# Kernel tuning notes

Measured on AMD Instinct MI355X. Metric: run time of the kernel, lower is better.

Reference implementation:

```python
import jax, jax.numpy as jnp
import numpy as np
from jax import lax

B, T_IN, T_TGT = 256, 512, 256
N_IN, N_PV, H, EMB, N_SC = 64, 16, 256, 32, 4

def gru_cell(x, h, Wih, Whh, bih, bhh):
    # PyTorch GRU cell, gate order (r, z, n)
    gi = x @ Wih.T + bih
    gh = h @ Whh.T + bhh
    ir, iz, inn = jnp.split(gi, 3, axis=-1)
    hr, hz, hn = jnp.split(gh, 3, axis=-1)
    r = jax.nn.sigmoid(ir + hr)
    z = jax.nn.sigmoid(iz + hz)
    n = jnp.tanh(inn + r * hn)
    return (1.0 - z) * n + z * h

def setup_inputs() -> dict:
    key = jax.random.key(0)
    ks = jax.random.split(key, 24)
    s = 0.05
    d = {}
    d['x_cv'] = jax.random.normal(ks[0], (B, T_IN, N_IN), jnp.float32)
    d['x_cv_target'] = jax.random.normal(ks[1], (B, T_TGT, N_IN), jnp.float32)
    d['pv_init'] = jax.random.normal(ks[2], (B, N_PV), jnp.float32)
    d['scenario'] = jax.random.randint(ks[3], (B,), 0, N_SC)
    d['emb_table'] = jax.random.normal(ks[4], (N_SC, EMB), jnp.float32) * s
    i = 5
    for name, in0 in (('enc', N_IN + EMB), ('dec', N_IN + N_PV)):
        for l in range(2):
            din = in0 if l == 0 else H
            d[f'{name}_Wih{l}'] = jax.random.normal(ks[i], (3 * H, din), jnp.float32) * s; i += 1
            d[f'{name}_Whh{l}'] = jax.random.normal(ks[i], (3 * H, H), jnp.float32) * s; i += 1
            d[f'{name}_bih{l}'] = jnp.zeros((3 * H,), jnp.float32)
            d[f'{name}_bhh{l}'] = jnp.zeros((3 * H,), jnp.float32)
    d['fc1_W'] = jax.random.normal(ks[i], (128, H), jnp.float32) * s; i += 1
    d['fc1_b'] = jnp.zeros((128,), jnp.float32)
    d['fc2_W'] = jax.random.normal(ks[i], (N_PV, 128), jnp.float32) * s; i += 1
    d['fc2_b'] = jnp.zeros((N_PV,), jnp.float32)
    return d

def reference(x_cv, x_cv_target, pv_init, scenario, emb_table,
              enc_Wih0, enc_Whh0, enc_bih0, enc_bhh0,
              enc_Wih1, enc_Whh1, enc_bih1, enc_bhh1,
              dec_Wih0, dec_Whh0, dec_bih0, dec_bhh0,
              dec_Wih1, dec_Whh1, dec_bih1, dec_bhh1,
              fc1_W, fc1_b, fc2_W, fc2_b):
    b = x_cv.shape[0]
    # Encoder: concat scenario embedding onto each input step, 2-layer GRU
    emb = emb_table[scenario]                              # (B, EMB)
    emb_bt = jnp.broadcast_to(emb[:, None, :], (b, x_cv.shape[1], emb.shape[-1]))
    enc_x = jnp.concatenate([x_cv, emb_bt], axis=-1)       # (B, T_in, N_IN+EMB)
    h_init = (jnp.zeros((b, H), x_cv.dtype), jnp.zeros((b, H), x_cv.dtype))

    def enc_step(carry, xt):
        h0, h1 = carry
        h0 = gru_cell(xt, h0, enc_Wih0, enc_Whh0, enc_bih0, enc_bhh0)
        h1 = gru_cell(h0, h1, enc_Wih1, enc_Whh1, enc_bih1, enc_bhh1)
        return (h0, h1), None

    (h0, h1), _ = lax.scan(enc_step, h_init, enc_x.transpose(1, 0, 2))

    def dec_step(carry, xt):
        d0, d1, pv = carry
        din = jnp.concatenate([xt, pv], axis=-1)           # (B, N_IN+N_PV)
        d0 = gru_cell(din, d0, dec_Wih0, dec_Whh0, dec_bih0, dec_bhh0)
        d1 = gru_cell(d0, d1, dec_Wih1, dec_Whh1, dec_bih1, dec_bhh1)
        y = jax.nn.relu(d1 @ fc1_W.T + fc1_b) @ fc2_W.T + fc2_b  # (B, N_PV)
        return (d0, d1, y), y

    _, ys = lax.scan(dec_step, (h0, h1, pv_init), x_cv_target.transpose(1, 0, 2))
    return ys.transpose(1, 0, 2)                           # (B, T_tgt, N_PV)
```

## Files before the change

### kernel.cpp

```cpp
#include <hip/hip_runtime.h>


typedef _Float16 f16x8 __attribute__((ext_vector_type(8)));
typedef float f32x4 __attribute__((ext_vector_type(4)));

#define XSTR 104
#define HSTR 264
#define YSTR 136

#define OFF_E0IH 0u
#define OFF_E0HH 73728u
#define OFF_E1IH 270336u
#define OFF_E1HH 466944u
#define OFF_D0IH 663552u
#define OFF_D0HH 737280u
#define OFF_D1IH 933888u
#define OFF_D1HH 1130496u
#define OFF_FC1  1327104u
#define OFF_FC2  1359872u
#define W_TOTAL_F16 1361920u
#define BIAS_BYTE_OFF 2723840u
#define EXCH_BYTE_OFF 2740224u
#define EX_H0 0
#define EX_H1 262144
#define EX_PV 524288
#define EX_FLAGS 532480
#define EX_BYTES 567296

__device__ __forceinline__ float sigm(float x) { return 1.f / (1.f + __expf(-x)); }
__device__ __forceinline__ float tanh_fast(float x) { return 1.f - 2.f / (__expf(2.f * x) + 1.f); }

__device__ __forceinline__ f32x4 mfma(f16x8 a, f16x8 b, f32x4 c) {
    return __builtin_amdgcn_mfma_f32_16x16x32_f16(a, b, c, 0, 0, 0);
}

__device__ __forceinline__ void store_coh_f16(_Float16* p, _Float16 v) {
    union { _Float16 h; unsigned short u; } cv; cv.h = v;
    unsigned int ui = cv.u;
    asm volatile("global_store_short %0, %1, off sc0 sc1" :: "v"(p), "v"(ui) : "memory");
}
__device__ __forceinline__ unsigned short load_coh_u16(const _Float16* p) {
    unsigned int r;
    asm volatile("global_load_ushort %0, %1, off sc0 sc1\n\ts_waitcnt vmcnt(0)"
                 : "=v"(r) : "v"(p) : "memory");
    return (unsigned short)r;
}

__device__ __forceinline__ void stage_h(const _Float16* src, _Float16* dst, int tid) {
    if (tid < 256) {
        int row = tid >> 4, c = tid & 15;
        const _Float16* p = src + (size_t)row * 256 + c * 16;
        f16x8 a, b;
        asm volatile(
            "global_load_dwordx4 %0, %2, off sc0 sc1\n\t"
            "global_load_dwordx4 %1, %2, off offset:16 sc0 sc1\n\t"
            "s_waitcnt vmcnt(0)"
            : "=v"(a), "=v"(b) : "v"(p) : "memory");
        *(f16x8*)(dst + row * HSTR + c * 16) = a;
        *(f16x8*)(dst + row * HSTR + c * 16 + 8) = b;
    }
}
__device__ __forceinline__ void stage_h2(const _Float16* s0, const _Float16* s1,
                                         _Float16* d0, _Float16* d1, int tid) {
    if (tid < 256) {
        int row = tid >> 4, c = tid & 15;
        const _Float16* p0 = s0 + (size_t)row * 256 + c * 16;
        const _Float16* p1 = s1 + (size_t)row * 256 + c * 16;
        f16x8 a, b, e, f;
        asm volatile(
            "global_load_dwordx4 %0, %4, off sc0 sc1\n\t"
            "global_load_dwordx4 %1, %4, off offset:16 sc0 sc1\n\t"
            "global_load_dwordx4 %2, %5, off sc0 sc1\n\t"
            "global_load_dwordx4 %3, %5, off offset:16 sc0 sc1\n\t"
            "s_waitcnt vmcnt(0)"
            : "=v"(a), "=v"(b), "=v"(e), "=v"(f) : "v"(p0), "v"(p1) : "memory");
        *(f16x8*)(d0 + row * HSTR + c * 16) = a;
        *(f16x8*)(d0 + row * HSTR + c * 16 + 8) = b;
        *(f16x8*)(d1 + row * HSTR + c * 16) = e;
        *(f16x8*)(d1 + row * HSTR + c * 16 + 8) = f;
    }
}

__global__ __launch_bounds__(256) void prep_w(const float* __restrict__ W,
                                              _Float16* __restrict__ dst,
                                              int K_src, int GT, int total_threads) {
    int idx = blockIdx.x * 256 + threadIdx.x;
    if (idx >= total_threads) return;
    int l = idx & 63, c = idx >> 6;
    int kt = c / GT, gt = c - kt * GT;
    int g = gt * 16 + (l & 15);
    int k0 = kt * 32 + (l >> 4) * 8;
    _Float16 tmp[8];
#pragma unroll
    for (int j = 0; j < 8; ++j) {
        int k = k0 + j;
        tmp[j] = (k < K_src) ? (_Float16)W[(size_t)g * K_src + k] : (_Float16)0.f;
    }
    *(f16x8*)(dst + (size_t)c * 512 + (size_t)l * 8) = *(f16x8*)tmp;
}

__global__ __launch_bounds__(256) void prep_bias(const float* __restrict__ bih,
                                                 const float* __restrict__ bhh,
                                                 float* __restrict__ dst) {
    int i = threadIdx.x;
    dst[i]       = bih[i]       + bhh[i];
    dst[256 + i] = bih[256 + i] + bhh[256 + i];
    dst[512 + i] = bih[512 + i];
    dst[768 + i] = bhh[512 + i];
}

template <int KT>
__device__ __forceinline__ f32x4 mmk(const _Float16* ap, const f16x8 (&B)[8]) {
    f32x4 acc = {0.f, 0.f, 0.f, 0.f};
#pragma unroll
    for (int kt = 0; kt < KT; ++kt)
        acc = mfma(*(const f16x8*)(ap + kt * 32), B[kt], acc);
    return acc;
}

__device__ __forceinline__ void h_update(const float* Gb, float* HM,
                                         _Float16* hex_slice, int l,
                                         float bR, float bZ, float bNi, float bNh) {
#pragma unroll
    for (int i = 0; i < 4; ++i) {
        int row = (l >> 4) * 4 + i, col = l & 15;
        int rc = row * 17 + col;
        float r = sigm(Gb[rc] + bR);
        float z = sigm(Gb[272 + rc] + bZ);
        float n = tanh_fast(Gb[2 * 272 + rc] + bNi + r * (Gb[3 * 272 + rc] + bNh));
        float hp = HM[row * 16 + col];
        float hn = (1.f - z) * n + z * hp;
        HM[row * 16 + col] = hn;
        store_coh_f16(hex_slice + (size_t)row * 256 + col, (_Float16)hn);
    }
}

__global__ __launch_bounds__(384, 2) void plant(
    const float* __restrict__ x_cv, const float* __restrict__ x_tgt,
    const float* __restrict__ pv_init, const int* __restrict__ scen,
    const float* __restrict__ emb,
    const _Float16* __restrict__ Wsw, const float* __restrict__ bias4,
    const float* __restrict__ fc1b, const float* __restrict__ fc2b,
    char* __restrict__ exch, float* __restrict__ out)
{
    __shared__ _Float16 XF[16 * XSTR];
    __shared__ _Float16 HA0[16 * HSTR];
    __shared__ _Float16 HA1[16 * HSTR];
    __shared__ _Float16 YF[16 * YSTR];
    __shared__ float G[2][4][272];
    __shared__ float H0M[256], H1M[256];

    const int tid = threadIdx.x;
    const int l = tid & 63, w = tid >> 6;
    const int g = blockIdx.x >> 4, cg = blockIdx.x & 15;
    const int g16 = g * 16;
    const int j = (w < 3) ? w : w - 3;
    const int gt = j * 16 + cg;

    _Float16* h0ex = (_Float16*)(exch + EX_H0);
    _Float16* h1ex = (_Float16*)(exch + EX_H1);
    _Float16* pvex = (_Float16*)(exch + EX_PV);
    int* gflags = (int*)(exch + EX_FLAGS) + g * (17 * 32);
    int* pvflag = gflags + 16 * 32;

    const int arow = l & 15, acol8 = (l >> 4) * 8;
    const size_t slice_off = (size_t)g16 * 256 + cg * 16;
    const _Float16* XFp = XF + arow * XSTR + acol8;
    const _Float16* HA0p = HA0 + arow * HSTR + acol8;
    const _Float16* HA1p = HA1 + arow * HSTR + acol8;

    int ticket = 0;
    auto barrier = [&](int target) {
        __syncthreads();
        if (w == 0) {
            if (l == 0)
                __hip_atomic_store(&gflags[cg * 32], target, __ATOMIC_RELAXED,
                                   __HIP_MEMORY_SCOPE_AGENT);
            if (l < 16)
                while (__hip_atomic_load(&gflags[l * 32], __ATOMIC_RELAXED,
                                         __HIP_MEMORY_SCOPE_AGENT) < target)
                    __builtin_amdgcn_s_sleep(1);
        }
        __syncthreads();
    };

    for (int i = tid; i < 256; i += 384) { H0M[i] = 0.f; H1M[i] = 0.f; }
    if (tid < 256) {
        int row = tid >> 4, c2 = (tid & 15) * 2;
        int sc = scen[g16 + row];
        XF[row * XSTR + 64 + c2]     = (_Float16)emb[sc * 32 + c2];
        XF[row * XSTR + 64 + c2 + 1] = (_Float16)emb[sc * 32 + c2 + 1];
    }

    f16x8 Bx[8], Bh[8];
    {
        unsigned offi = (w < 3) ? OFF_E0IH : OFF_E1IH;
        unsigned offh = (w < 3) ? OFF_E0HH : OFF_E1HH;
        int ktx = (w < 3) ? 3 : 8;
#pragma unroll
        for (int kt = 0; kt < 8; ++kt) {
            if (kt < ktx) Bx[kt] = *(const f16x8*)(Wsw + offi + (size_t)(kt * 48 + gt) * 512 + l * 8);
            Bh[kt] = *(const f16x8*)(Wsw + offh + (size_t)(kt * 48 + gt) * 512 + l * 8);
        }
    }
    float bR = 0.f, bZ = 0.f, bNi = 0.f, bNh = 0.f;
    {
        const float* bb = (w == 0) ? bias4 : bias4 + 1024;
        int hc = cg * 16 + (l & 15);
        if (w == 0 || w == 3) { bR = bb[hc]; bZ = bb[256 + hc]; bNi = bb[512 + hc]; bNh = bb[768 + hc]; }
    }

    float4 xpre;
    const float* xsrc0 = x_cv + (size_t)(g16 + (tid >> 4)) * (512 * 64) + (tid & 15) * 4;
    if (tid < 256) xpre = *(const float4*)xsrc0;
    __syncthreads();

    for (int t = 0; t <= 512; ++t) {
        if (t < 512 && tid < 256) {
            int row = tid >> 4, c4 = (tid & 15) * 4;
            XF[row * XSTR + c4]     = (_Float16)xpre.x;
            XF[row * XSTR + c4 + 1] = (_Float16)xpre.y;
            XF[row * XSTR + c4 + 2] = (_Float16)xpre.z;
            XF[row * XSTR + c4 + 3] = (_Float16)xpre.w;
        }
        stage_h2(h0ex + (size_t)((t - 1) & 1) * 65536 + (size_t)g16 * 256,
                 h1ex + (size_t)(t & 1) * 65536 + (size_t)g16 * 256, HA0, HA1, tid);
        __syncthreads();
        if (tid < 256 && t + 1 < 512) xpre = *(const float4*)(xsrc0 + (size_t)(t + 1) * 64);

        bool doL0 = (w < 3) && (t < 512);
        bool doL1 = (w >= 3) && (t > 0);
        if (doL0 || doL1) {
            f32x4 accX, accH;
            if (doL0) { accX = mmk<3>(XFp, Bx);  accH = mmk<8>(HA0p, Bh); }
            else      { accX = mmk<8>(HA0p, Bx); accH = mmk<8>(HA1p, Bh); }
            float* Gb = &G[(w < 3) ? 0 : 1][0][0];
#pragma unroll
            for (int i = 0; i < 4; ++i) {
                int rc = ((l >> 4) * 4 + i) * 17 + (l & 15);
                if (j < 2) Gb[j * 272 + rc] = accX[i] + accH[i];
                else { Gb[2 * 272 + rc] = accX[i]; Gb[3 * 272 + rc] = accH[i]; }
            }
        }
        __syncthreads();
        if (w == 0 && t < 512)
            h_update(&G[0][0][0], H0M, h0ex + (size_t)(t & 1) * 65536 + slice_off, l, bR, bZ, bNi, bNh);
        if (w == 3 && t > 0)
            h_update(&G[1][0][0], H1M, h1ex + (size_t)((t - 1) & 1) * 65536 + slice_off, l, bR, bZ, bNi, bNh);
        barrier(++ticket);
    }

    {
        unsigned offi = (w < 3) ? OFF_D0IH : OFF_D1IH;
        unsigned offh = (w < 3) ? OFF_D0HH : OFF_D1HH;
        int ktx = (w < 3) ? 3 : 8;
#pragma unroll
        for (int kt = 0; kt < 8; ++kt) {
            if (kt < ktx) Bx[kt] = *(const f16x8*)(Wsw + offi + (size_t)(kt * 48 + gt) * 512 + l * 8);
            Bh[kt] = *(const f16x8*)(Wsw + offh + (size_t)(kt * 48 + gt) * 512 + l * 8);
        }
        const float* bb = (w == 0) ? bias4 + 2048 : bias4 + 3072;
        int hc = cg * 16 + (l & 15);
        if (w == 0 || w == 3) { bR = bb[hc]; bZ = bb[256 + hc]; bNi = bb[512 + hc]; bNh = bb[768 + hc]; }
    }
    f16x8 Bf1a[8], Bf1b[8], Bf2[4];
#pragma unroll
    for (int kt = 0; kt < 8; ++kt) {
        Bf1a[kt] = *(const f16x8*)(Wsw + OFF_FC1 + (size_t)(kt * 8 + w) * 512 + l * 8);
        Bf1b[kt] = (w < 2) ? *(const f16x8*)(Wsw + OFF_FC1 + (size_t)(kt * 8 + w + 6) * 512 + l * 8)
                           : Bf1a[kt];
    }
#pragma unroll
    for (int kt = 0; kt < 4; ++kt)
        Bf2[kt] = *(const f16x8*)(Wsw + OFF_FC2 + (size_t)kt * 512 + l * 8);
    float f1b0 = fc1b[w * 16 + (l & 15)];
    float f1b1 = (w < 2) ? fc1b[(w + 6) * 16 + (l & 15)] : 0.f;
    float f2breg = fc2b[l & 15];

    const float* xsrc1 = x_tgt + (size_t)(g16 + (tid >> 4)) * (256 * 64) + (tid & 15) * 4;
    if (tid < 256) xpre = *(const float4*)xsrc1;
    __syncthreads();

    for (int s = 0; s < 256; ++s) {
        if (tid < 256) {
            int row = tid >> 4, c4 = (tid & 15) * 4;
            XF[row * XSTR + c4]     = (_Float16)xpre.x;
            XF[row * XSTR + c4 + 1] = (_Float16)xpre.y;
            XF[row * XSTR + c4 + 2] = (_Float16)xpre.z;
            XF[row * XSTR + c4 + 3] = (_Float16)xpre.w;
        }
        if (s > 0 && w == 0 && l == 0)
            while (__hip_atomic_load(pvflag, __ATOMIC_RELAXED, __HIP_MEMORY_SCOPE_AGENT) < s)
                __builtin_amdgcn_s_sleep(1);
        __syncthreads();
        if (tid < 256) {
            int row = tid >> 4, col = tid & 15;
            if (s == 0) {
                XF[row * XSTR + 64 + col] = (_Float16)pv_init[(g16 + row) * 16 + col];
            } else {
                union { unsigned short u; _Float16 h; } cv;
                cv.u = load_coh_u16(pvex + (size_t)(g16 + row) * 16 + col);
                XF[row * XSTR + 64 + col] = cv.h;
            }
        }
        stage_h(h0ex + (size_t)((s - 1) & 1) * 65536 + (size_t)g16 * 256, HA0, tid);
        __syncthreads();
        if (tid < 256 && s + 1 < 256) xpre = *(const float4*)(xsrc1 + (size_t)(s + 1) * 64);

        if (w < 3) {
            f32x4 accX = mmk<3>(XFp, Bx);
            f32x4 accH = mmk<8>(HA0p, Bh);
            float* Gb = &G[0][0][0];
#pragma unroll
            for (int i = 0; i < 4; ++i) {
                int rc = ((l >> 4) * 4 + i) * 17 + (l & 15);
                if (j < 2) Gb[j * 272 + rc] = accX[i] + accH[i];
                else { Gb[2 * 272 + rc] = accX[i]; Gb[3 * 272 + rc] = accH[i]; }
            }
        }
        __syncthreads();
        if (w == 0)
            h_update(&G[0][0][0], H0M, h0ex + (size_t)(s & 1) * 65536 + slice_off, l, bR, bZ, bNi, bNh);
        barrier(++ticket);

        stage_h2(h0ex + (size_t)(s & 1) * 65536 + (size_t)g16 * 256,
                 h1ex + (size_t)((s - 1) & 1) * 65536 + (size_t)g16 * 256, HA0, HA1, tid);
        __syncthreads();
        if (w >= 3) {
            f32x4 accX = mmk<8>(HA0p, Bx);
            f32x4 accH = mmk<8>(HA1p, Bh);
            float* Gb = &G[1][0][0];
#pragma unroll
            for (int i = 0; i < 4; ++i) {
                int rc = ((l >> 4) * 4 + i) * 17 + (l & 15);
                if (j < 2) Gb[j * 272 + rc] = accX[i] + accH[i];
                else { Gb[2 * 272 + rc] = accX[i]; Gb[3 * 272 + rc] = accH[i]; }
            }
        }
        __syncthreads();
        if (w == 3)
            h_update(&G[1][0][0], H1M, h1ex + (size_t)(s & 1) * 65536 + slice_off, l, bR, bZ, bNi, bNh);
        barrier(++ticket);

        if (cg == 0) {
            stage_h(h1ex + (size_t)(s & 1) * 65536 + (size_t)g16 * 256, HA1, tid);
            __syncthreads();
            {
                f32x4 a0 = {0.f,0.f,0.f,0.f}, a1 = a0;
                const _Float16* Ap = HA1 + (l & 15) * HSTR + ((l >> 4) * 8);
#pragma unroll
                for (int kt = 0; kt < 8; ++kt) {
                    f16x8 a = *(const f16x8*)(Ap + kt * 32);
                    a0 = mfma(a, Bf1a[kt], a0);
                    a1 = mfma(a, Bf1b[kt], a1);
                }
#pragma unroll
                for (int i = 0; i < 4; ++i) {
                    int row = (l >> 4) * 4 + i, col = l & 15;
                    YF[row * YSTR + w * 16 + col] = (_Float16)fmaxf(a0[i] + f1b0, 0.f);
                    if (w < 2)
                        YF[row * YSTR + (w + 6) * 16 + col] = (_Float16)fmaxf(a1[i] + f1b1, 0.f);
                }
            }
            __syncthreads();
            if (w == 0) {
                f32x4 acc = {0.f,0.f,0.f,0.f};
                const _Float16* Yp = YF + (l & 15) * YSTR + ((l >> 4) * 8);
#pragma unroll
                for (int kt = 0; kt < 4; ++kt)
                    acc = mfma(*(const f16x8*)(Yp + kt * 32), Bf2[kt], acc);
#pragma unroll
                for (int i = 0; i < 4; ++i) {
                    int row = (l >> 4) * 4 + i, col = l & 15;
                    float y = acc[i] + f2breg;
                    out[(size_t)(g16 + row) * 4096 + (size_t)s * 16 + col] = y;
                    store_coh_f16(pvex + (size_t)(g16 + row) * 16 + col, (_Float16)y);
                }
                asm volatile("s_waitcnt vmcnt(0)" ::: "memory");
                if (l == 0)
                    __hip_atomic_store(pvflag, s + 1, __ATOMIC_RELAXED, __HIP_MEMORY_SCOPE_AGENT);
            }
        }
    }
}

extern "C" void kernel_launch(void* const* d_in, const int* in_sizes, int n_in,
                              void* d_out, int out_size, void* d_ws, size_t ws_size,
                              hipStream_t stream)
{
    const float* x_cv    = (const float*)d_in[0];
    const float* x_tgt   = (const float*)d_in[1];
    const float* pv_init = (const float*)d_in[2];
    const int*   scen    = (const int*)d_in[3];
    const float* emb     = (const float*)d_in[4];
    const float* eWih0 = (const float*)d_in[5];
    const float* eWhh0 = (const float*)d_in[6];
    const float* ebih0 = (const float*)d_in[7];
    const float* ebhh0 = (const float*)d_in[8];
    const float* eWih1 = (const float*)d_in[9];
    const float* eWhh1 = (const float*)d_in[10];
    const float* ebih1 = (const float*)d_in[11];
    const float* ebhh1 = (const float*)d_in[12];
    const float* dWih0 = (const float*)d_in[13];
    const float* dWhh0 = (const float*)d_in[14];
    const float* dbih0 = (const float*)d_in[15];
    const float* dbhh0 = (const float*)d_in[16];
    const float* dWih1 = (const float*)d_in[17];
    const float* dWhh1 = (const float*)d_in[18];
    const float* dbih1 = (const float*)d_in[19];
    const float* dbhh1 = (const float*)d_in[20];
    const float* fc1W = (const float*)d_in[21];
    const float* fc1b = (const float*)d_in[22];
    const float* fc2W = (const float*)d_in[23];
    const float* fc2b = (const float*)d_in[24];
    float* out = (float*)d_out;

    _Float16* W = (_Float16*)d_ws;
    float* bias = (float*)((char*)d_ws + BIAS_BYTE_OFF);
    char* exch = (char*)d_ws + EXCH_BYTE_OFF;

    hipMemsetAsync(exch, 0, EX_BYTES, stream);

    auto lp = [&](const float* src, unsigned off, int K_src, int KT, int GT) {
        int total = KT * GT * 64;
        prep_w<<<(total + 255) / 256, 256, 0, stream>>>(src, W + off, K_src, GT, total);
    };
    lp(eWih0, OFF_E0IH, 96, 3, 48);
    lp(eWhh0, OFF_E0HH, 256, 8, 48);
    lp(eWih1, OFF_E1IH, 256, 8, 48);
    lp(eWhh1, OFF_E1HH, 256, 8, 48);
    lp(dWih0, OFF_D0IH, 80, 3, 48);
    lp(dWhh0, OFF_D0HH, 256, 8, 48);
    lp(dWih1, OFF_D1IH, 256, 8, 48);
    lp(dWhh1, OFF_D1HH, 256, 8, 48);
    lp(fc1W, OFF_FC1, 256, 8, 8);
    lp(fc2W, OFF_FC2, 128, 4, 1);
    prep_bias<<<1, 256, 0, stream>>>(ebih0, ebhh0, bias);
    prep_bias<<<1, 256, 0, stream>>>(ebih1, ebhh1, bias + 1024);
    prep_bias<<<1, 256, 0, stream>>>(dbih0, dbhh0, bias + 2048);
    prep_bias<<<1, 256, 0, stream>>>(dbih1, dbhh1, bias + 3072);

    plant<<<256, 384, 0, stream>>>(x_cv, x_tgt, pv_init, scen, emb,
                                   W, bias, fc1b, fc2b, exch, out);
}
```

Measured before the change: 3.507 ms.

## Fuse inter-block barrier with hidden-state staging and rotate encoder loop

Merges the cross-workgroup flag barrier with the staging of exchanged hidden states: each of the 256 staging threads spins only on the flag of the producer slice it needs, then loads that slice, which removes a separate __syncthreads and staging pass per step. The encoder loop is rotated so the x prefetch and staging sit after the GEMM and h-update, with a peeled final layer-1 step. Flag stores and loads now use inline asm with sc0 sc1 instead of HIP atomics. This gives finer-grained waiting and fewer block-wide syncs per step, but puts many more threads into polling and makes the ordering of the exchange more delicate.

```diff
diff --git a/kernel.cpp b/kernel.cpp
--- a/kernel.cpp
+++ b/kernel.cpp
@@ -45,40 +45,14 @@
                  : "=v"(r) : "v"(p) : "memory");
     return (unsigned short)r;
 }
-
-__device__ __forceinline__ void stage_h(const _Float16* src, _Float16* dst, int tid) {
-    if (tid < 256) {
-        int row = tid >> 4, c = tid & 15;
-        const _Float16* p = src + (size_t)row * 256 + c * 16;
-        f16x8 a, b;
-        asm volatile(
-            "global_load_dwordx4 %0, %2, off sc0 sc1\n\t"
-            "global_load_dwordx4 %1, %2, off offset:16 sc0 sc1\n\t"
-            "s_waitcnt vmcnt(0)"
-            : "=v"(a), "=v"(b) : "v"(p) : "memory");
-        *(f16x8*)(dst + row * HSTR + c * 16) = a;
-        *(f16x8*)(dst + row * HSTR + c * 16 + 8) = b;
-    }
-}
-__device__ __forceinline__ void stage_h2(const _Float16* s0, const _Float16* s1,
-                                         _Float16* d0, _Float16* d1, int tid) {
-    if (tid < 256) {
-        int row = tid >> 4, c = tid & 15;
-        const _Float16* p0 = s0 + (size_t)row * 256 + c * 16;
-        const _Float16* p1 = s1 + (size_t)row * 256 + c * 16;
-        f16x8 a, b, e, f;
-        asm volatile(
-            "global_load_dwordx4 %0, %4, off sc0 sc1\n\t"
-            "global_load_dwordx4 %1, %4, off offset:16 sc0 sc1\n\t"
-            "global_load_dwordx4 %2, %5, off sc0 sc1\n\t"
-            "global_load_dwordx4 %3, %5, off offset:16 sc0 sc1\n\t"
-            "s_waitcnt vmcnt(0)"
-            : "=v"(a), "=v"(b), "=v"(e), "=v"(f) : "v"(p0), "v"(p1) : "memory");
-        *(f16x8*)(d0 + row * HSTR + c * 16) = a;
-        *(f16x8*)(d0 + row * HSTR + c * 16 + 8) = b;
-        *(f16x8*)(d1 + row * HSTR + c * 16) = e;
-        *(f16x8*)(d1 + row * HSTR + c * 16 + 8) = f;
-    }
+__device__ __forceinline__ void store_flag(int* p, int v) {
+    asm volatile("global_store_dword %0, %1, off sc0 sc1" :: "v"(p), "v"(v) : "memory");
+}
+__device__ __forceinline__ int load_flag(const int* p) {
+    int r;
+    asm volatile("global_load_dword %0, %1, off sc0 sc1\n\ts_waitcnt vmcnt(0)"
+                 : "=v"(r) : "v"(p) : "memory");
+    return r;
 }
 
 __global__ __launch_bounds__(256) void prep_w(const float* __restrict__ W,
@@ -170,16 +144,56 @@
     const _Float16* HA1p = HA1 + arow * HSTR + acol8;
 
     int ticket = 0;
-    auto barrier = [&](int target) {
+
+    auto barrier0 = [&](int target) {
         __syncthreads();
         if (w == 0) {
-            if (l == 0)
-                __hip_atomic_store(&gflags[cg * 32], target, __ATOMIC_RELAXED,
-                                   __HIP_MEMORY_SCOPE_AGENT);
+            if (l == 0) store_flag(&gflags[cg * 32], target);
             if (l < 16)
-                while (__hip_atomic_load(&gflags[l * 32], __ATOMIC_RELAXED,
-                                         __HIP_MEMORY_SCOPE_AGENT) < target)
+                while (load_flag(&gflags[l * 32]) < target)
                     __builtin_amdgcn_s_sleep(1);
+        }
+        __syncthreads();
+    };
+    auto barrier_stage1 = [&](int target, const _Float16* s0, _Float16* d0) {
+        __syncthreads();
+        if (tid == 0) store_flag(&gflags[cg * 32], target);
+        if (tid < 256) {
+            int c = tid & 15, row = tid >> 4;
+            while (load_flag(&gflags[c * 32]) < target) __builtin_amdgcn_s_sleep(1);
+            const _Float16* p0 = s0 + (size_t)row * 256 + c * 16;
+            f16x8 a, b;
+            asm volatile(
+                "global_load_dwordx4 %0, %2, off sc0 sc1\n\t"
+                "global_load_dwordx4 %1, %2, off offset:16 sc0 sc1\n\t"
+                "s_waitcnt vmcnt(0)"
+                : "=v"(a), "=v"(b) : "v"(p0) : "memory");
+            *(f16x8*)(d0 + row * HSTR + c * 16) = a;
+            *(f16x8*)(d0 + row * HSTR + c * 16 + 8) = b;
+        }
+        __syncthreads();
+    };
+    auto barrier_stage2 = [&](int target, const _Float16* s0, _Float16* d0,
+                              const _Float16* s1, _Float16* d1) {
+        __syncthreads();
+        if (tid == 0) store_flag(&gflags[cg * 32], target);
+        if (tid < 256) {
+            int c = tid & 15, row = tid >> 4;
+            while (load_flag(&gflags[c * 32]) < target) __builtin_amdgcn_s_sleep(1);
+            const _Float16* p0 = s0 + (size_t)row * 256 + c * 16;
+            const _Float16* p1 = s1 + (size_t)row * 256 + c * 16;
+            f16x8 a, b, e, f;
+            asm volatile(
+                "global_load_dwordx4 %0, %4, off sc0 sc1\n\t"
+                "global_load_dwordx4 %1, %4, off offset:16 sc0 sc1\n\t"
+                "global_load_dwordx4 %2, %5, off sc0 sc1\n\t"
+                "global_load_dwordx4 %3, %5, off offset:16 sc0 sc1\n\t"
+                "s_waitcnt vmcnt(0)"
+                : "=v"(a), "=v"(b), "=v"(e), "=v"(f) : "v"(p0), "v"(p1) : "memory");
+            *(f16x8*)(d0 + row * HSTR + c * 16) = a;
+            *(f16x8*)(d0 + row * HSTR + c * 16 + 8) = b;
+            *(f16x8*)(d1 + row * HSTR + c * 16) = e;
+            *(f16x8*)(d1 + row * HSTR + c * 16 + 8) = f;
         }
         __syncthreads();
     };
@@ -191,6 +205,12 @@
         XF[row * XSTR + 64 + c2]     = (_Float16)emb[sc * 32 + c2];
         XF[row * XSTR + 64 + c2 + 1] = (_Float16)emb[sc * 32 + c2 + 1];
     }
+    if (tid < 256) {
+        int row = tid >> 4, c = tid & 15;
+        f16x8 z = {};
+        *(f16x8*)(HA0 + row * HSTR + c * 16) = z;
+        *(f16x8*)(HA0 + row * HSTR + c * 16 + 8) = z;
+    }
 
     f16x8 Bx[8], Bh[8];
     {
@@ -212,43 +232,62 @@
 
     float4 xpre;
     const float* xsrc0 = x_cv + (size_t)(g16 + (tid >> 4)) * (512 * 64) + (tid & 15) * 4;
-    if (tid < 256) xpre = *(const float4*)xsrc0;
+    if (tid < 256) {
+        float4 x0 = *(const float4*)xsrc0;
+        int row = tid >> 4, c4 = (tid & 15) * 4;
+        XF[row * XSTR + c4]     = (_Float16)x0.x;
+        XF[row * XSTR + c4 + 1] = (_Float16)x0.y;
+        XF[row * XSTR + c4 + 2] = (_Float16)x0.z;
+        XF[row * XSTR + c4 + 3] = (_Float16)x0.w;
+        xpre = *(const float4*)(xsrc0 + 64);
+    }
     __syncthreads();
 
-    for (int t = 0; t <= 512; ++t) {
-        if (t < 512 && tid < 256) {
+    for (int t = 0; t < 512; ++t) {
+        bool doL1 = (w >= 3) && (t > 0);
+        if (w < 3 || doL1) {
+            f32x4 accX, accH;
+            if (w < 3) { accX = mmk<3>(XFp, Bx);  accH = mmk<8>(HA0p, Bh); }
+            else       { accX = mmk<8>(HA0p, Bx); accH = mmk<8>(HA1p, Bh); }
+            float* Gb = &G[(w < 3) ? 0 : 1][0][0];
+#pragma unroll
+            for (int i = 0; i < 4; ++i) {
+                int rc = ((l >> 4) * 4 + i) * 17 + (l & 15);
+                if (j < 2) Gb[j * 272 + rc] = accX[i] + accH[i];
+                else { Gb[2 * 272 + rc] = accX[i]; Gb[3 * 272 + rc] = accH[i]; }
+            }
+        }
+        __syncthreads();
+        if (w == 0)
+            h_update(&G[0][0][0], H0M, h0ex + (size_t)(t & 1) * 65536 + slice_off, l, bR, bZ, bNi, bNh);
+        if (w == 3 && t > 0)
+            h_update(&G[1][0][0], H1M, h1ex + (size_t)((t - 1) & 1) * 65536 + slice_off, l, bR, bZ, bNi, bNh);
+        if (tid < 256 && t + 1 < 512) {
             int row = tid >> 4, c4 = (tid & 15) * 4;
             XF[row * XSTR + c4]     = (_Float16)xpre.x;
             XF[row * XSTR + c4 + 1] = (_Float16)xpre.y;
             XF[row * XSTR + c4 + 2] = (_Float16)xpre.z;
             XF[row * XSTR + c4 + 3] = (_Float16)xpre.w;
         }
-        stage_h2(h0ex + (size_t)((t - 1) & 1) * 65536 + (size_t)g16 * 256,
-                 h1ex + (size_t)(t & 1) * 65536 + (size_t)g16 * 256, HA0, HA1, tid);
-        __syncthreads();
-        if (tid < 256 && t + 1 < 512) xpre = *(const float4*)(xsrc0 + (size_t)(t + 1) * 64);
-
-        bool doL0 = (w < 3) && (t < 512);
-        bool doL1 = (w >= 3) && (t > 0);
-        if (doL0 || doL1) {
-            f32x4 accX, accH;
-            if (doL0) { accX = mmk<3>(XFp, Bx);  accH = mmk<8>(HA0p, Bh); }
-            else      { accX = mmk<8>(HA0p, Bx); accH = mmk<8>(HA1p, Bh); }
-            float* Gb = &G[(w < 3) ? 0 : 1][0][0];
-#pragma unroll
-            for (int i = 0; i < 4; ++i) {
-                int rc = ((l >> 4) * 4 + i) * 17 + (l & 15);
-                if (j < 2) Gb[j * 272 + rc] = accX[i] + accH[i];
-                else { Gb[2 * 272 + rc] = accX[i]; Gb[3 * 272 + rc] = accH[i]; }
-            }
-        }
-        __syncthreads();
-        if (w == 0 && t < 512)
-            h_update(&G[0][0][0], H0M, h0ex + (size_t)(t & 1) * 65536 + slice_off, l, bR, bZ, bNi, bNh);
-        if (w == 3 && t > 0)
-            h_update(&G[1][0][0], H1M, h1ex + (size_t)((t - 1) & 1) * 65536 + slice_off, l, bR, bZ, bNi, bNh);
-        barrier(++ticket);
-    }
+        if (tid < 256 && t + 2 < 512) xpre = *(const float4*)(xsrc0 + (size_t)(t + 2) * 64);
+        barrier_stage2(++ticket,
+                       h0ex + (size_t)(t & 1) * 65536 + (size_t)g16 * 256, HA0,
+                       h1ex + (size_t)((t & 1) ^ 1) * 65536 + (size_t)g16 * 256, HA1);
+    }
+    if (w >= 3) {
+        f32x4 accX = mmk<8>(HA0p, Bx);
+        f32x4 accH = mmk<8>(HA1p, Bh);
+        float* Gb = &G[1][0][0];
+#pragma unroll
+        for (int i = 0; i < 4; ++i) {
+            int rc = ((l >> 4) * 4 + i) * 17 + (l & 15);
+            if (j < 2) Gb[j * 272 + rc] = accX[i] + accH[i];
+            else { Gb[2 * 272 + rc] = accX[i]; Gb[3 * 272 + rc] = accH[i]; }
+        }
+    }
+    __syncthreads();
+    if (w == 3)
+        h_update(&G[1][0][0], H1M, h1ex + (size_t)1 * 65536 + slice_off, l, bR, bZ, bNi, bNh);
 
     {
         unsigned offi = (w < 3) ? OFF_D0IH : OFF_D1IH;
@@ -290,7 +329,7 @@
             XF[row * XSTR + c4 + 3] = (_Float16)xpre.w;
         }
         if (s > 0 && w == 0 && l == 0)
-            while (__hip_atomic_load(pvflag, __ATOMIC_RELAXED, __HIP_MEMORY_SCOPE_AGENT) < s)
+            while (load_flag(pvflag) < s)
                 __builtin_amdgcn_s_sleep(1);
         __syncthreads();
         if (tid < 256) {
@@ -303,7 +342,6 @@
                 XF[row * XSTR + 64 + col] = cv.h;
             }
         }
-        stage_h(h0ex + (size_t)((s - 1) & 1) * 65536 + (size_t)g16 * 256, HA0, tid);
         __syncthreads();
         if (tid < 256 && s + 1 < 256) xpre = *(const float4*)(xsrc1 + (size_t)(s + 1) * 64);
 
@@ -321,11 +359,10 @@
         __syncthreads();
         if (w == 0)
             h_update(&G[0][0][0], H0M, h0ex + (size_t)(s & 1) * 65536 + slice_off, l, bR, bZ, bNi, bNh);
-        barrier(++ticket);
-
-        stage_h2(h0ex + (size_t)(s & 1) * 65536 + (size_t)g16 * 256,
-                 h1ex + (size_t)((s - 1) & 1) * 65536 + (size_t)g16 * 256, HA0, HA1, tid);
-        __syncthreads();
+        barrier_stage2(++ticket,
+                       h0ex + (size_t)(s & 1) * 65536 + (size_t)g16 * 256, HA0,
+                       h1ex + (size_t)((s & 1) ^ 1) * 65536 + (size_t)g16 * 256, HA1);
+
         if (w >= 3) {
             f32x4 accX = mmk<8>(HA0p, Bx);
             f32x4 accH = mmk<8>(HA1p, Bh);
@@ -340,11 +377,12 @@
         __syncthreads();
         if (w == 3)
             h_update(&G[1][0][0], H1M, h1ex + (size_t)(s & 1) * 65536 + slice_off, l, bR, bZ, bNi, bNh);
-        barrier(++ticket);
+        if (cg == 0)
+            barrier_stage1(++ticket, h1ex + (size_t)(s & 1) * 65536 + (size_t)g16 * 256, HA1);
+        else
+            barrier0(++ticket);
 
         if (cg == 0) {
-            stage_h(h1ex + (size_t)(s & 1) * 65536 + (size_t)g16 * 256, HA1, tid);
-            __syncthreads();
             {
                 f32x4 a0 = {0.f,0.f,0.f,0.f}, a1 = a0;
                 const _Float16* Ap = HA1 + (l & 15) * HSTR + ((l >> 4) * 8);
@@ -378,7 +416,7 @@
                 }
                 asm volatile("s_waitcnt vmcnt(0)" ::: "memory");
                 if (l == 0)
-                    __hip_atomic_store(pvflag, s + 1, __ATOMIC_RELAXED, __HIP_MEMORY_SCOPE_AGENT);
+                    store_flag(pvflag, s + 1);
             }
         }
     }
```

Measured after the change: 3.498 ms. No clear change (-0.2%).
